# Optimization experiments

Hardware: AMD Instinct MI355X
Metric: run time of the kernel (lower is better)

The kernel has to match this reference:

```python
import jax, jax.numpy as jnp
import numpy as np

N_NODES = 4096
N_EDGES = 16384
L = 512
MP_STEPS = 5
DT = 0.01


def _mlp(x, W1, b1, W2, b2):
    return jax.nn.relu(x @ W1 + b1) @ W2 + b2


def _ln(x):
    m = jnp.mean(x, axis=-1, keepdims=True)
    v = jnp.var(x, axis=-1, keepdims=True)
    return (x - m) * jax.lax.rsqrt(v + 1e-6)


_PARAM_SHAPES = [
    ("enc_e_W1", (1, L)), ("enc_e_b1", (L,)), ("enc_e_W2", (L, L)), ("enc_e_b2", (L,)),
    ("enc_n_W1", (1, L)), ("enc_n_b1", (L,)), ("enc_n_W2", (L, L)), ("enc_n_b2", (L,)),
    ("proc_e_W1", (3 * L, L)), ("proc_e_b1", (L,)), ("proc_e_W2", (L, L)), ("proc_e_b2", (L,)),
    ("proc_n_W1", (2 * L, L)), ("proc_n_b1", (L,)), ("proc_n_W2", (L, L)), ("proc_n_b2", (L,)),
    ("dec_e_W1", (L, L)), ("dec_e_b1", (L,)), ("dec_e_W2", (L, 1)), ("dec_e_b2", (1,)),
]


def setup_inputs() -> dict:
    key = jax.random.key(0)
    ks = jax.random.split(key, 3 + len(_PARAM_SHAPES))
    d = {}
    d["state"] = jax.random.normal(ks[0], (N_EDGES + N_NODES,), dtype=jnp.float32)
    d["senders"] = jax.random.randint(ks[1], (N_EDGES,), 0, N_NODES)
    d["receivers"] = jax.random.randint(ks[2], (N_EDGES,), 0, N_NODES)
    for i, (name, shp) in enumerate(_PARAM_SHAPES):
        if name.endswith(("b1", "b2")):
            d[name] = jnp.zeros(shp, dtype=jnp.float32)
        else:
            d[name] = 0.02 * jax.random.normal(ks[3 + i], shp, dtype=jnp.float32)
    return d


def _hamiltonian(x, senders, receivers,
                 enc_e_W1, enc_e_b1, enc_e_W2, enc_e_b2,
                 enc_n_W1, enc_n_b1, enc_n_W2, enc_n_b2,
                 proc_e_W1, proc_e_b1, proc_e_W2, proc_e_b2,
                 proc_n_W1, proc_n_b1, proc_n_W2, proc_n_b2,
                 dec_e_W1, dec_e_b1, dec_e_W2, dec_e_b2):
    # graph_from_state: edge scalars then node scalars
    e = x[:N_EDGES].reshape(N_EDGES, 1)
    n = x[N_EDGES:].reshape(N_NODES, 1)
    # encode (MLP + layer norm)
    eh = _ln(_mlp(e, enc_e_W1, enc_e_b1, enc_e_W2, enc_e_b2))  # [E, L]
    nh = _ln(_mlp(n, enc_n_W1, enc_n_b1, enc_n_W2, enc_n_b2))  # [N, L]
    # process: num_mp_steps of GraphNetwork-style message passing, shared params
    for _ in range(MP_STEPS):
        msg_in = jnp.concatenate([eh, nh[senders], nh[receivers]], axis=-1)  # [E, 3L]
        eh = eh + _mlp(msg_in, proc_e_W1, proc_e_b1, proc_e_W2, proc_e_b2)
        agg = jax.ops.segment_sum(eh, receivers, num_segments=N_NODES)  # [N, L]
        node_in = jnp.concatenate([nh, agg], axis=-1)  # [N, 2L]
        nh = nh + _mlp(node_in, proc_n_W1, proc_n_b1, proc_n_W2, proc_n_b2)
    # decode edges to scalars; H = sum of decoded edge energies
    dec_e = _mlp(eh, dec_e_W1, dec_e_b1, dec_e_W2, dec_e_b2)  # [E, 1]
    return jnp.sum(dec_e)


def reference(state, senders, receivers,
              enc_e_W1, enc_e_b1, enc_e_W2, enc_e_b2,
              enc_n_W1, enc_n_b1, enc_n_W2, enc_n_b2,
              proc_e_W1, proc_e_b1, proc_e_W2, proc_e_b2,
              proc_n_W1, proc_n_b1, proc_n_W2, proc_n_b2,
              dec_e_W1, dec_e_b1, dec_e_W2, dec_e_b2):
    def H_fn(x):
        return _hamiltonian(x, senders, receivers,
                            enc_e_W1, enc_e_b1, enc_e_W2, enc_e_b2,
                            enc_n_W1, enc_n_b1, enc_n_W2, enc_n_b2,
                            proc_e_W1, proc_e_b1, proc_e_W2, proc_e_b2,
                            proc_n_W1, proc_n_b1, proc_n_W2, proc_n_b2,
                            dec_e_W1, dec_e_b1, dec_e_W2, dec_e_b2)
    H, dH = jax.value_and_grad(H_fn)(state)
    # one integrator step driven by the Hamiltonian gradient (stand-in for DAE solve)
    next_state = state - DT * dH
    return next_state
```

## Files before the change

### kernel.cpp

```cpp
#include <hip/hip_runtime.h>


#define E_ROWS 16384
#define N_ROWS 4096
#define ALL_ROWS 20480
#define DT_F   0.01f

typedef unsigned char u8;
typedef unsigned short u16;
typedef unsigned long long u64;
typedef __attribute__((ext_vector_type(8))) short short8v;
typedef __attribute__((ext_vector_type(4))) float f32x4;

__device__ __forceinline__ u16 f2b(float f) {
    union { float f; unsigned u; } v; v.f = f;
    unsigned r = v.u + 0x7FFF + ((v.u >> 16) & 1);
    return (u16)(r >> 16);
}
__device__ __forceinline__ float b2f(u16 u) {
    union { unsigned u; float f; } v; v.u = ((unsigned)u) << 16;
    return v.f;
}
__device__ __forceinline__ void gld16(const u16* g, u16* l) {
    __builtin_amdgcn_global_load_lds((const __attribute__((address_space(1))) void*)g,
                                     (__attribute__((address_space(3))) void*)l, 16, 0, 0);
}
template<int N> __device__ __forceinline__ void waitcnt_vm() {
    if constexpr (N == 0)      asm volatile("s_waitcnt vmcnt(0)" ::: "memory");
    else if constexpr (N == 2) asm volatile("s_waitcnt vmcnt(2)" ::: "memory");
    else if constexpr (N == 3) asm volatile("s_waitcnt vmcnt(3)" ::: "memory");
    else if constexpr (N == 4) asm volatile("s_waitcnt vmcnt(4)" ::: "memory");
    else if constexpr (N == 6) asm volatile("s_waitcnt vmcnt(6)" ::: "memory");
    else if constexpr (N == 8) asm volatile("s_waitcnt vmcnt(8)" ::: "memory");
}

template<int BM, int WM, int WN, int KTOT, int LDA, int LDC,
         bool ADD_C, bool GATHER2, bool BIAS, bool RELU_MASK, bool APPLY_MASK,
         bool WBF16, bool DUALOUT, bool ROWDOT, bool DECW2, bool BSEL>
__global__ __launch_bounds__(256)
void bgemm(const u16* __restrict__ A, const u16* __restrict__ Bt, const u16* __restrict__ Bt2,
           u16* __restrict__ Cb,
           const u16* __restrict__ Cinb, const float* __restrict__ bias,
           const float* __restrict__ bias2, const u16* __restrict__ G12b,
           const int* __restrict__ sidx, const int* __restrict__ ridx,
           u8* __restrict__ maskw, u16* __restrict__ C2b,
           const float* __restrict__ wvec, const float* __restrict__ wvec2,
           float* __restrict__ outp)
{
    constexpr int BN = WN * 64;
    constexpr int NA = BM / 16;
    constexpr int TC = (BM + BN) / 16;
    constexpr int PER = TC / 4;
    constexpr int NT = KTOT / 32;
    constexpr int IFRAG = BM / WM / 16;
    constexpr int BUFU = TC * 512;
    constexpr int LSZ = (3 * BUFU > BM * BN) ? 3 * BUFU : BM * BN;
    __shared__ u16 Ls[LSZ];

    const int tid = threadIdx.x;
    const int lane = tid & 63;
    const int wv = tid >> 6;
    const int wr = wv / WN;
    const int wc = wv % WN;

    const int gx = gridDim.x;
    int id = blockIdx.y * gx + blockIdx.x;
    const int nwg = gx * gridDim.y;
    id = (id & 7) * (nwg >> 3) + (id >> 3);
    const int bx = id % gx;
    const int by = id / gx;
    const int rowBase = by * BM;
    const int colBase = bx * BN;

    const u16* BtU = Bt;
    const float* biasU = bias;
    const float* wvecU = wvec;
    if (BSEL && rowBase >= E_ROWS) { BtU = Bt2; biasU = bias2; wvecU = wvec2; }

    const int srow = lane & 15;
    const int slotk = (lane >> 4) << 3;

    const u16* srcs[PER];
    int dstoff[PER];
#pragma unroll
    for (int q = 0; q < PER; ++q) {
        const int c = wv + (q << 2);
        if (c < NA)
            srcs[q] = A + (size_t)(rowBase + c * 16 + srow) * LDA + slotk;
        else
            srcs[q] = BtU + (size_t)(colBase + (c - NA) * 16 + srow) * KTOT + slotk;
        dstoff[q] = c * 512;
    }

    f32x4 acc[IFRAG][4];
#pragma unroll
    for (int i = 0; i < IFRAG; ++i)
#pragma unroll
        for (int j = 0; j < 4; ++j)
            acc[i][j] = (f32x4){0.f, 0.f, 0.f, 0.f};

    const int fro = ((lane >> 4) << 7) + ((lane & 15) << 3);

#pragma unroll
    for (int q = 0; q < PER; ++q) gld16(srcs[q], &Ls[dstoff[q]]);
#pragma unroll
    for (int q = 0; q < PER; ++q) gld16(srcs[q] + 32, &Ls[BUFU + dstoff[q]]);
    waitcnt_vm<PER>();
    __builtin_amdgcn_s_barrier();
    asm volatile("" ::: "memory");

    for (int t = 0; t < NT; ++t) {
        const int cur = t % 3;
        if (t + 2 < NT) {
            const int nxt = (t + 2) % 3;
#pragma unroll
            for (int q = 0; q < PER; ++q)
                gld16(srcs[q] + (t + 2) * 32, &Ls[nxt * BUFU + dstoff[q]]);
        }
        const u16* Lc = &Ls[cur * BUFU];
        short8v af[IFRAG], bfm[4];
#pragma unroll
        for (int i = 0; i < IFRAG; ++i)
            af[i] = *(const short8v*)&Lc[((wr * IFRAG + i) << 9) + fro];
#pragma unroll
        for (int j = 0; j < 4; ++j)
            bfm[j] = *(const short8v*)&Lc[((NA + (wc << 2) + j) << 9) + fro];
#pragma unroll
        for (int i = 0; i < IFRAG; ++i)
#pragma unroll
            for (int j = 0; j < 4; ++j)
                acc[i][j] = __builtin_amdgcn_mfma_f32_16x16x32_bf16(af[i], bfm[j], acc[i][j], 0, 0, 0);
        if (t + 1 < NT) {
            if (t + 2 < NT) waitcnt_vm<PER>();
            else            waitcnt_vm<0>();
            __builtin_amdgcn_s_barrier();
            asm volatile("" ::: "memory");
        }
    }
    __syncthreads();

    {
        const int colL = wc * 64 + (lane & 15);
        const int rowL0 = wr * (BM / WM) + ((lane >> 4) << 2);
#pragma unroll
        for (int i = 0; i < IFRAG; ++i)
#pragma unroll
            for (int r = 0; r < 4; ++r) {
                const int row = rowL0 + (i << 4) + r;
#pragma unroll
                for (int j = 0; j < 4; ++j) {
                    const int col = colL + (j << 4);
                    int byte = row * (BN * 2) + col * 2;
                    byte ^= (row & 7) << 4;
                    *(u16*)((char*)Ls + byte) = f2b(acc[i][j][r]);
                }
            }
        __syncthreads();

        constexpr int TPR = BN / 8;
        constexpr int RPP = 256 / TPR;
        constexpr int NP = BM / RPP;
        const int rloc = tid / TPR;
        const int seg = tid % TPR;
        const int col0 = seg * 8;
        const bool upper = DUALOUT && (colBase >= 512);
#pragma unroll
        for (int p = 0; p < NP; ++p) {
            const int row = p * RPP + rloc;
            const int grow = rowBase + row;
            const int gcol = colBase + col0;
            int byte = row * (BN * 2) + col0 * 2;
            byte ^= (row & 7) << 4;
            const short8v sv = *(const short8v*)((const char*)Ls + byte);
            float v[8];
#pragma unroll
            for (int e = 0; e < 8; ++e) v[e] = b2f((u16)sv[e]);

            if (DUALOUT && upper) {
                short8v res;
#pragma unroll
                for (int e = 0; e < 8; ++e) res[e] = (short)f2b(v[e]);
                *(short8v*)&C2b[(size_t)grow * 512 + (gcol - 512)] = res;
                continue;
            }
            if (GATHER2) {
                const int si = sidx[grow], ri = ridx[grow];
                const short8v g1 = *(const short8v*)&G12b[(size_t)si * 1024 + gcol];
                const short8v g2 = *(const short8v*)&G12b[(size_t)ri * 1024 + 512 + gcol];
#pragma unroll
                for (int e = 0; e < 8; ++e) v[e] += b2f((u16)g1[e]) + b2f((u16)g2[e]);
            }
            if (ADD_C) {
                const short8v c8 = *(const short8v*)&Cinb[(size_t)grow * LDC + gcol];
#pragma unroll
                for (int e = 0; e < 8; ++e) v[e] += b2f((u16)c8[e]);
            }
            if (BIAS) {
                const float4 b0 = *(const float4*)&biasU[gcol];
                const float4 b1 = *(const float4*)&biasU[gcol + 4];
                v[0] += b0.x; v[1] += b0.y; v[2] += b0.z; v[3] += b0.w;
                v[4] += b1.x; v[5] += b1.y; v[6] += b1.z; v[7] += b1.w;
            }
            if (DECW2) {
                const float4 w0 = *(const float4*)&wvecU[gcol];
                const float4 w1 = *(const float4*)&wvecU[gcol + 4];
                const float wl[8] = {w0.x, w0.y, w0.z, w0.w, w1.x, w1.y, w1.z, w1.w};
                short8v res;
#pragma unroll
                for (int e = 0; e < 8; ++e) res[e] = (v[e] > 0.f) ? (short)f2b(wl[e]) : (short)0;
                *(short8v*)&Cb[(size_t)grow * LDC + gcol] = res;
                continue;
            }
            if (RELU_MASK) {
                u64 mm = 0;
#pragma unroll
                for (int e = 0; e < 8; ++e) {
                    const bool m = v[e] > 0.f;
                    mm |= (u64)(m ? 1 : 0) << (e * 8);
                    if (!m) v[e] = 0.f;
                }
                *(u64*)&maskw[(size_t)grow * 512 + gcol] = mm;
            }
            if (APPLY_MASK) {
                const u64 mm = *(const u64*)&maskw[(size_t)grow * 512 + gcol];
#pragma unroll
                for (int e = 0; e < 8; ++e)
                    if (!((mm >> (e * 8)) & 0xff)) v[e] = 0.f;
            }
            if (ROWDOT) {
                const float4 w0 = *(const float4*)&wvecU[gcol];
                const float4 w1 = *(const float4*)&wvecU[gcol + 4];
                float rds = v[0] * w0.x + v[1] * w0.y + v[2] * w0.z + v[3] * w0.w
                          + v[4] * w1.x + v[5] * w1.y + v[6] * w1.z + v[7] * w1.w;
#pragma unroll
                for (int m = 1; m < TPR; m <<= 1) rds += __shfl_xor(rds, m);
                if (seg == 0) atomicAdd(outp + grow, -DT_F * rds);
            }
            if (WBF16) {
                short8v res;
#pragma unroll
                for (int e = 0; e < 8; ++e) res[e] = (short)f2b(v[e]);
                *(short8v*)&Cb[(size_t)grow * LDC + gcol] = res;
            }
        }
    }
}

struct WArgs {
    const float* src[10];
    u16* dstP[10];
    u16* dstT[10];
    int ldP[10], ldT[10];
};

__global__ void wcvt_kernel(WArgs a)
{
    const int i = blockIdx.z;
    const float* W = a.src[i];
    u16* P = a.dstP[i]; const int lp = a.ldP[i];
    u16* T = a.dstT[i]; const int lt = a.ldT[i];
    __shared__ u16 t[64][66];
    const int rb = blockIdx.y << 6, cb = blockIdx.x << 6;
    const int tr = threadIdx.x >> 4;
    const int tc = (threadIdx.x & 15) << 2;
#pragma unroll
    for (int rr = 0; rr < 4; ++rr) {
        const int r = tr + (rr << 4);
        const float4 v = *(const float4*)&W[(size_t)(rb + r) * 512 + cb + tc];
        ushort4 u; u.x = f2b(v.x); u.y = f2b(v.y); u.z = f2b(v.z); u.w = f2b(v.w);
        *(ushort4*)&P[(size_t)(rb + r) * lp + cb + tc] = u;
        t[r][tc] = u.x; t[r][tc + 1] = u.y; t[r][tc + 2] = u.z; t[r][tc + 3] = u.w;
    }
    __syncthreads();
#pragma unroll
    for (int rr = 0; rr < 4; ++rr) {
        const int n = tr + (rr << 4);
        ushort4 u;
        u.x = t[tc][n]; u.y = t[tc + 1][n]; u.z = t[tc + 2][n]; u.w = t[tc + 3][n];
        *(ushort4*)&T[(size_t)(cb + n) * lt + rb + tc] = u;
    }
}

__device__ void csr_build(const int* __restrict__ idx, int* __restrict__ starts,
                          int* __restrict__ eids)
{
    __shared__ int hist[4096];
    __shared__ int scanbuf[1024];
    const int t = threadIdx.x;
    for (int i = t; i < 4096; i += 1024) hist[i] = 0;
    __syncthreads();
    for (int e = t; e < 16384; e += 1024) atomicAdd(&hist[idx[e]], 1);
    __syncthreads();
    const int base = t << 2;
    const int l0 = hist[base], l1 = hist[base + 1], l2 = hist[base + 2], l3 = hist[base + 3];
    const int lsum = l0 + l1 + l2 + l3;
    scanbuf[t] = lsum;
    __syncthreads();
    for (int ofs = 1; ofs < 1024; ofs <<= 1) {
        const int v = scanbuf[t];
        const int u = (t >= ofs) ? scanbuf[t - ofs] : 0;
        __syncthreads();
        scanbuf[t] = v + u;
        __syncthreads();
    }
    const int excl = scanbuf[t] - lsum;
    const int p0 = excl, p1 = p0 + l0, p2 = p1 + l1, p3 = p2 + l2;
    starts[base] = p0; starts[base + 1] = p1; starts[base + 2] = p2; starts[base + 3] = p3;
    if (t == 0) starts[4096] = 16384;
    __syncthreads();
    hist[base] = p0; hist[base + 1] = p1; hist[base + 2] = p2; hist[base + 3] = p3;
    __syncthreads();
    for (int e = t; e < 16384; e += 1024) {
        const int pos = atomicAdd(&hist[idx[e]], 1);
        eids[pos] = e;
    }
    __syncthreads();
    for (int n = t; n < 4096; n += 1024) {
        const int s0 = starts[n], s1 = hist[n];
        for (int i = s0 + 1; i < s1; ++i) {
            const int v = eids[i];
            int j = i - 1;
            while (j >= s0 && eids[j] > v) { eids[j + 1] = eids[j]; --j; }
            eids[j + 1] = v;
        }
    }
}

__global__ __launch_bounds__(1024) void csr2_kernel(const int* __restrict__ senders,
                                                    const int* __restrict__ receivers,
                                                    int* __restrict__ sst, int* __restrict__ seid,
                                                    int* __restrict__ rst, int* __restrict__ reid)
{
    if (blockIdx.x == 0) csr_build(receivers, rst, reid);
    else                 csr_build(senders, sst, seid);
}

__global__ void init_out_kernel(const float* __restrict__ state, float* __restrict__ out)
{
    const int t = blockIdx.x * 256 + threadIdx.x;
    out[t] = state[t];
}

__global__ void seg_agg_fwd_kernel(const u16* __restrict__ ehb, const int* __restrict__ starts,
                                   const int* __restrict__ eids, const u16* __restrict__ nhb,
                                   u16* __restrict__ nagg)
{
    const int n = blockIdx.x, c = threadIdx.x;
    const int s0 = starts[n], s1 = starts[n + 1];
    float a0 = 0.f, a1 = 0.f;
    for (int i = s0; i < s1; ++i) {
        const u16* p = ehb + (size_t)eids[i] * 512;
        a0 += b2f(p[c]); a1 += b2f(p[c + 256]);
    }
    u16* d = nagg + (size_t)n * 1024;
    const u16* s = nhb + (size_t)n * 512;
    d[c] = s[c]; d[c + 256] = s[c + 256];
    d[512 + c] = f2b(a0); d[768 + c] = f2b(a1);
}

__global__ void seg_sr_bwd_kernel(const u16* __restrict__ dh1e,
                                  const int* __restrict__ sst, const int* __restrict__ seid,
                                  const int* __restrict__ rst, const int* __restrict__ reid,
                                  u16* __restrict__ SR)
{
    const int n = blockIdx.x, c = threadIdx.x;
    float a0 = 0.f, a1 = 0.f, b0 = 0.f, b1 = 0.f;
    for (int i = sst[n]; i < sst[n + 1]; ++i) {
        const u16* p = dh1e + (size_t)seid[i] * 512;
        a0 += b2f(p[c]); a1 += b2f(p[c + 256]);
    }
    for (int i = rst[n]; i < rst[n + 1]; ++i) {
        const u16* p = dh1e + (size_t)reid[i] * 512;
        b0 += b2f(p[c]); b1 += b2f(p[c + 256]);
    }
    u16* d = SR + (size_t)n * 1024;
    d[c] = f2b(a0); d[c + 256] = f2b(a1);
    d[512 + c] = f2b(b0); d[768 + c] = f2b(b1);
}

__global__ void enc_h1_kernel(const float* __restrict__ x,
                              const float* __restrict__ W1e, const float* __restrict__ b1e,
                              const float* __restrict__ W1n, const float* __restrict__ b1n,
                              u16* __restrict__ h1b, u8* __restrict__ mask)
{
    const int idx = blockIdx.x * 256 + threadIdx.x;
    const int row = idx >> 7;
    const int c = (idx & 127) << 2;
    const bool edge = row < E_ROWS;
    const float* W1 = edge ? W1e : W1n;
    const float* b1 = edge ? b1e : b1n;
    const float xv = x[row];
    const float4 w = *(const float4*)&W1[c];
    const float4 b = *(const float4*)&b1[c];
    float4 v;
    v.x = fmaf(xv, w.x, b.x); v.y = fmaf(xv, w.y, b.y);
    v.z = fmaf(xv, w.z, b.z); v.w = fmaf(xv, w.w, b.w);
    uchar4 m;
    m.x = v.x > 0.f; m.y = v.y > 0.f; m.z = v.z > 0.f; m.w = v.w > 0.f;
    v.x = m.x ? v.x : 0.f; v.y = m.y ? v.y : 0.f;
    v.z = m.z ? v.z : 0.f; v.w = m.w ? v.w : 0.f;
    const size_t o = (size_t)row * 512 + c;
    ushort4 u; u.x = f2b(v.x); u.y = f2b(v.y); u.z = f2b(v.z); u.w = f2b(v.w);
    *(ushort4*)&h1b[o] = u;
    *(uchar4*)&mask[o] = m;
}

__global__ void ln_fwd_kernel(u16* __restrict__ x, u16* __restrict__ xhat_b,
                              float* __restrict__ rstd_save)
{
    const int row = blockIdx.x, tid = threadIdx.x;
    u16* p = x + (size_t)row * 512;
    const float a = b2f(p[tid]), b = b2f(p[tid + 256]);
    __shared__ float s1[256], s2[256];
    s1[tid] = a + b; s2[tid] = a * a + b * b;
    __syncthreads();
    for (int d = 128; d > 0; d >>= 1) {
        if (tid < d) { s1[tid] += s1[tid + d]; s2[tid] += s2[tid + d]; }
        __syncthreads();
    }
    const float mean = s1[0] * (1.f / 512.f);
    const float var = s2[0] * (1.f / 512.f) - mean * mean;
    const float r = rsqrtf(var + 1e-6f);
    const u16 ya = f2b((a - mean) * r), yb = f2b((b - mean) * r);
    p[tid] = ya; p[tid + 256] = yb;
    xhat_b[(size_t)row * 512 + tid] = ya;
    xhat_b[(size_t)row * 512 + tid + 256] = yb;
    if (tid == 0) rstd_save[row] = r;
}

__global__ void ln_bwd_kernel(u16* __restrict__ d, const u16* __restrict__ xhat_b,
                              const float* __restrict__ rstd)
{
    const int row = blockIdx.x, tid = threadIdx.x;
    u16* p = d + (size_t)row * 512;
    const u16* xh = xhat_b + (size_t)row * 512;
    const float da = b2f(p[tid]), dbv = b2f(p[tid + 256]);
    const float xa = b2f(xh[tid]), xbv = b2f(xh[tid + 256]);
    __shared__ float s1[256], s2[256];
    s1[tid] = da + dbv; s2[tid] = da * xa + dbv * xbv;
    __syncthreads();
    for (int dd = 128; dd > 0; dd >>= 1) {
        if (tid < dd) { s1[tid] += s1[tid + dd]; s2[tid] += s2[tid + dd]; }
        __syncthreads();
    }
    const float m1 = s1[0] * (1.f / 512.f);
    const float m2 = s2[0] * (1.f / 512.f);
    const float r = rstd[row];
    p[tid] = f2b(r * (da - m1 - xa * m2));
    p[tid + 256] = f2b(r * (dbv - m1 - xbv * m2));
}

__global__ void gather_add_kernel(u16* __restrict__ dst, const u16* __restrict__ src,
                                  const int* __restrict__ idx)
{
    const int t = blockIdx.x * 256 + threadIdx.x;
    const int row = t >> 6;
    const int c = (t & 63) << 3;
    const size_t o = (size_t)row * 512 + c;
    short8v a = *(const short8v*)&dst[o];
    const short8v g = *(const short8v*)&src[(size_t)idx[row] * 512 + c];
    short8v r;
#pragma unroll
    for (int i = 0; i < 8; ++i)
        r[i] = (short)f2b(b2f((u16)a[i]) + b2f((u16)g[i]));
    *(short8v*)&dst[o] = r;
}

extern "C" void kernel_launch(void* const* d_in, const int* in_sizes, int n_in,
                              void* d_out, int out_size, void* d_ws, size_t ws_size,
                              hipStream_t stream)
{
    (void)in_sizes; (void)n_in; (void)out_size; (void)ws_size;
    const float* state     = (const float*)d_in[0];
    const int*   senders   = (const int*)d_in[1];
    const int*   receivers = (const int*)d_in[2];
    const float* enc_e_W1 = (const float*)d_in[3];
    const float* enc_e_b1 = (const float*)d_in[4];
    const float* enc_e_W2 = (const float*)d_in[5];
    const float* enc_e_b2 = (const float*)d_in[6];
    const float* enc_n_W1 = (const float*)d_in[7];
    const float* enc_n_b1 = (const float*)d_in[8];
    const float* enc_n_W2 = (const float*)d_in[9];
    const float* enc_n_b2 = (const float*)d_in[10];
    const float* pe_W1 = (const float*)d_in[11];
    const float* pe_b1 = (const float*)d_in[12];
    const float* pe_W2 = (const float*)d_in[13];
    const float* pe_b2 = (const float*)d_in[14];
    const float* pn_W1 = (const float*)d_in[15];
    const float* pn_b1 = (const float*)d_in[16];
    const float* pn_W2 = (const float*)d_in[17];
    const float* pn_b2 = (const float*)d_in[18];
    const float* de_W1 = (const float*)d_in[19];
    const float* de_b1 = (const float*)d_in[20];
    const float* de_W2 = (const float*)d_in[21];
    float* out = (float*)d_out;

    const size_t EL = (size_t)E_ROWS * 512, NL = (size_t)N_ROWS * 512;
    const size_t AL = (size_t)ALL_ROWS * 512;
    const size_t LL = 512 * 512;
    char* w = (char*)d_ws;
    size_t off = 0;
    auto carve = [&](size_t bytes) -> char* {
        char* p = w + off;
        off += (bytes + 255) & ~(size_t)255;
        return p;
    };
    u16* wb = (u16*)carve(20 * LL * 2);
    u16* WT0 = wb;           u16* WT1 = wb + LL;      u16* WT2 = wb + 2 * LL;
    u16* WT34 = wb + 3 * LL;                          u16* WT5 = wb + 5 * LL;
    u16* WT8 = wb + 6 * LL;  u16* WT9 = wb + 7 * LL;
    u16* WP0 = wb + 8 * LL;  u16* WP1 = wb + 9 * LL;  u16* WP2 = wb + 10 * LL;
    u16* WP5 = wb + 11 * LL; u16* WP8 = wb + 12 * LL; u16* WP9 = wb + 13 * LL;
    u16* WT67 = wb + 14 * LL;
    u16* WP34c = wb + 16 * LL;
    u16* WP67 = wb + 18 * LL;

    u16* ehb   = (u16*)carve(EL * 2);
    u16* nhb   = (u16*)carve(NL * 2);
    u16* h1eb  = (u16*)carve(EL * 2);
    u16* h1nb  = (u16*)carve(NL * 2);
    u16* eh0b  = (u16*)carve(EL * 2);
    u16* nh0b  = (u16*)carve(NL * 2);
    u8* menc   = (u8*)carve(AL);
    u16* G1b   = (u16*)carve(NL * 2);
    u16* G12b  = (u16*)carve(NL * 2 * 2);
    u16* nsr   = (u16*)carve(NL * 2 * 2);
    float* rstd = (float*)carve(ALL_ROWS * 4);
    u8* mpe    = (u8*)carve(5 * EL);
    u8* mpn    = (u8*)carve(5 * NL);
    int* rst  = (int*)carve(4097 * 4);
    int* reid = (int*)carve(16384 * 4);
    int* sst  = (int*)carve(4097 * 4);
    int* seid = (int*)carve(16384 * 4);

    const dim3 blk(256);
    const dim3 gE(4, E_ROWS / 128);
    const dim3 gA(4, ALL_ROWS / 128);
    const dim3 gN512(8, N_ROWS / 64);
    const dim3 gN1024(16, N_ROWS / 64);
    const float* fp = nullptr;
    u16* up = nullptr;
    const u16* cup = nullptr;
    const int* ip = nullptr;
    u8* mp = nullptr;
    float* f2p = nullptr;

    WArgs wa;
    const float* wsrc[10] = { enc_e_W2, enc_n_W2, pe_W1, pe_W1 + LL, pe_W1 + 2 * LL,
                              pe_W2, pn_W1, pn_W1 + LL, pn_W2, de_W1 };
    u16* dstP[10] = { WP0, WP1, WP2, WP34c, WP34c + 512, WP5, WP67, WP67 + LL, WP8, WP9 };
    int  ldP [10] = { 512, 512, 512, 1024,  1024,        512, 512,  512,       512, 512 };
    u16* dstT[10] = { WT0, WT1, WT2, WT34, WT34 + LL, WT5, WT67, WT67 + 512, WT8, WT9 };
    int  ldT [10] = { 512, 512, 512, 512,  512,       512, 1024, 1024,       512, 512 };
    for (int i = 0; i < 10; ++i) {
        wa.src[i] = wsrc[i]; wa.dstP[i] = dstP[i]; wa.dstT[i] = dstT[i];
        wa.ldP[i] = ldP[i]; wa.ldT[i] = ldT[i];
    }
    wcvt_kernel<<<dim3(8, 8, 10), blk, 0, stream>>>(wa);

    csr2_kernel<<<2, 1024, 0, stream>>>(senders, receivers, sst, seid, rst, reid);
    init_out_kernel<<<ALL_ROWS / 256, blk, 0, stream>>>(state, out);

    enc_h1_kernel<<<ALL_ROWS * 128 / 256, blk, 0, stream>>>(state, enc_e_W1, enc_e_b1,
                                                            enc_n_W1, enc_n_b1, h1eb, menc);
    bgemm<128,2,2,512,512,512, false,false,true,false,false, true,false,false,false,true>
        <<<gA, blk, 0, stream>>>(h1eb, WT0, WT1, ehb, cup, enc_e_b2, enc_n_b2, cup, ip, ip, mp, up, fp, fp, f2p);
    ln_fwd_kernel<<<ALL_ROWS, blk, 0, stream>>>(ehb, eh0b, rstd);

    for (int k = 0; k < 5; ++k) {
        bgemm<64,4,1,512,512,1024, false,false,false,false,false, true,false,false,false,false>
            <<<gN1024, blk, 0, stream>>>(nhb, WT34, cup, G12b, cup, fp, fp, cup, ip, ip, mp, up, fp, fp, f2p);
        bgemm<128,2,2,512,512,512, false,true,true,true,false, true,false,false,false,false>
            <<<gE, blk, 0, stream>>>(ehb, WT2, cup, h1eb, cup, pe_b1, fp, G12b, senders, receivers, mpe + (size_t)k * EL, up, fp, fp, f2p);
        bgemm<128,2,2,512,512,512, true,false,true,false,false, true,false,false,false,false>
            <<<gE, blk, 0, stream>>>(h1eb, WT5, cup, ehb, ehb, pe_b2, fp, cup, ip, ip, mp, up, fp, fp, f2p);
        seg_agg_fwd_kernel<<<N_ROWS, blk, 0, stream>>>(ehb, rst, reid, nhb, nsr);
        bgemm<64,4,1,1024,1024,512, false,false,true,true,false, true,false,false,false,false>
            <<<gN512, blk, 0, stream>>>(nsr, WT67, cup, h1nb, cup, pn_b1, fp, cup, ip, ip, mpn + (size_t)k * NL, up, fp, fp, f2p);
        bgemm<64,4,1,512,512,512, true,false,true,false,false, true,false,false,false,false>
            <<<gN512, blk, 0, stream>>>(h1nb, WT8, cup, nhb, nhb, pn_b2, fp, cup, ip, ip, mp, up, fp, fp, f2p);
    }

    bgemm<128,2,2,512,512,512, false,false,true,false,false, false,false,false,true,false>
        <<<gE, blk, 0, stream>>>(ehb, WT9, cup, h1eb, cup, de_b1, fp, cup, ip, ip, mp, up, de_W2, fp, f2p);

    bgemm<128,2,2,512,512,512, false,false,false,false,false, true,false,false,false,false>
        <<<gE, blk, 0, stream>>>(h1eb, WP9, cup, ehb, cup, fp, fp, cup, ip, ip, mp, up, fp, fp, f2p);

    for (int k = 4; k >= 0; --k) {
        if (k < 4) {
            bgemm<64,4,1,512,512,512, false,false,false,false,true, true,false,false,false,false>
                <<<gN512, blk, 0, stream>>>(nhb, WP8, cup, h1nb, cup, fp, fp, cup, ip, ip, mpn + (size_t)k * NL, up, fp, fp, f2p);
            bgemm<64,4,1,512,512,512, true,false,false,false,false, true,true,false,false,false>
                <<<gN1024, blk, 0, stream>>>(h1nb, WP67, cup, nhb, nhb, fp, fp, cup, ip, ip, mp, G1b, fp, fp, f2p);
            gather_add_kernel<<<E_ROWS * 64 / 256, blk, 0, stream>>>(ehb, G1b, receivers);
        }
        bgemm<128,2,2,512,512,512, false,false,false,false,true, true,false,false,false,false>
            <<<gE, blk, 0, stream>>>(ehb, WP5, cup, h1eb, cup, fp, fp, cup, ip, ip, mpe + (size_t)k * EL, up, fp, fp, f2p);
        bgemm<128,2,2,512,512,512, true,false,false,false,false, true,false,false,false,false>
            <<<gE, blk, 0, stream>>>(h1eb, WP2, cup, ehb, ehb, fp, fp, cup, ip, ip, mp, up, fp, fp, f2p);
        seg_sr_bwd_kernel<<<N_ROWS, blk, 0, stream>>>(h1eb, sst, seid, rst, reid, nsr);
        if (k == 4)
            bgemm<64,4,1,1024,1024,512, false,false,false,false,false, true,false,false,false,false>
                <<<gN512, blk, 0, stream>>>(nsr, WP34c, cup, nhb, cup, fp, fp, cup, ip, ip, mp, up, fp, fp, f2p);
        else
            bgemm<64,4,1,1024,1024,512, true,false,false,false,false, true,false,false,false,false>
                <<<gN512, blk, 0, stream>>>(nsr, WP34c, cup, nhb, nhb, fp, fp, cup, ip, ip, mp, up, fp, fp, f2p);
    }

    ln_bwd_kernel<<<ALL_ROWS, blk, 0, stream>>>(ehb, eh0b, rstd);
    bgemm<128,2,2,512,512,512, false,false,false,false,true, false,false,true,false,true>
        <<<gA, blk, 0, stream>>>(ehb, WP0, WP1, up, cup, fp, fp, cup, ip, ip, menc, up, enc_e_W1, enc_n_W1, out);
}
```

Baseline: 1.241 ms.

## Give each wave private double-buffered LDS tiles and drop per-step block barriers

```diff
diff --git a/kernel.cpp b/kernel.cpp
--- a/kernel.cpp
+++ b/kernel.cpp
@@ -27,10 +27,7 @@
 }
 template<int N> __device__ __forceinline__ void waitcnt_vm() {
     if constexpr (N == 0)      asm volatile("s_waitcnt vmcnt(0)" ::: "memory");
-    else if constexpr (N == 2) asm volatile("s_waitcnt vmcnt(2)" ::: "memory");
-    else if constexpr (N == 3) asm volatile("s_waitcnt vmcnt(3)" ::: "memory");
-    else if constexpr (N == 4) asm volatile("s_waitcnt vmcnt(4)" ::: "memory");
-    else if constexpr (N == 6) asm volatile("s_waitcnt vmcnt(6)" ::: "memory");
+    else if constexpr (N == 5) asm volatile("s_waitcnt vmcnt(5)" ::: "memory");
     else if constexpr (N == 8) asm volatile("s_waitcnt vmcnt(8)" ::: "memory");
 }
 
@@ -48,13 +45,12 @@
            float* __restrict__ outp)
 {
     constexpr int BN = WN * 64;
-    constexpr int NA = BM / 16;
-    constexpr int TC = (BM + BN) / 16;
-    constexpr int PER = TC / 4;
+    constexpr int NAW = BM / WM / 16;
+    constexpr int PERW = NAW + 4;
+    constexpr int WBUF = PERW * 512;
     constexpr int NT = KTOT / 32;
-    constexpr int IFRAG = BM / WM / 16;
-    constexpr int BUFU = TC * 512;
-    constexpr int LSZ = (3 * BUFU > BM * BN) ? 3 * BUFU : BM * BN;
+    constexpr int IFRAG = NAW;
+    constexpr int LSZ = (8 * WBUF > BM * BN) ? 8 * WBUF : BM * BN;
     __shared__ u16 Ls[LSZ];
 
     const int tid = threadIdx.x;
@@ -80,17 +76,15 @@
     const int srow = lane & 15;
     const int slotk = (lane >> 4) << 3;
 
-    const u16* srcs[PER];
-    int dstoff[PER];
-#pragma unroll
-    for (int q = 0; q < PER; ++q) {
-        const int c = wv + (q << 2);
-        if (c < NA)
-            srcs[q] = A + (size_t)(rowBase + c * 16 + srow) * LDA + slotk;
+    const u16* srcs[PERW];
+#pragma unroll
+    for (int q = 0; q < PERW; ++q) {
+        if (q < NAW)
+            srcs[q] = A + (size_t)(rowBase + wr * (BM / WM) + q * 16 + srow) * LDA + slotk;
         else
-            srcs[q] = BtU + (size_t)(colBase + (c - NA) * 16 + srow) * KTOT + slotk;
-        dstoff[q] = c * 512;
-    }
+            srcs[q] = BtU + (size_t)(colBase + wc * 64 + (q - NAW) * 16 + srow) * KTOT + slotk;
+    }
+    u16* Lw = Ls + wv * 2 * WBUF;
 
     f32x4 acc[IFRAG][4];
 #pragma unroll
@@ -102,40 +96,31 @@
     const int fro = ((lane >> 4) << 7) + ((lane & 15) << 3);
 
 #pragma unroll
-    for (int q = 0; q < PER; ++q) gld16(srcs[q], &Ls[dstoff[q]]);
-#pragma unroll
-    for (int q = 0; q < PER; ++q) gld16(srcs[q] + 32, &Ls[BUFU + dstoff[q]]);
-    waitcnt_vm<PER>();
-    __builtin_amdgcn_s_barrier();
-    asm volatile("" ::: "memory");
+    for (int q = 0; q < PERW; ++q) gld16(srcs[q], Lw + q * 512);
 
     for (int t = 0; t < NT; ++t) {
-        const int cur = t % 3;
-        if (t + 2 < NT) {
-            const int nxt = (t + 2) % 3;
-#pragma unroll
-            for (int q = 0; q < PER; ++q)
-                gld16(srcs[q] + (t + 2) * 32, &Ls[nxt * BUFU + dstoff[q]]);
+        if (t + 1 < NT) {
+            u16* Ln = Lw + ((t + 1) & 1) * WBUF;
+#pragma unroll
+            for (int q = 0; q < PERW; ++q)
+                gld16(srcs[q] + (t + 1) * 32, Ln + q * 512);
+            waitcnt_vm<PERW>();
+        } else {
+            waitcnt_vm<0>();
         }
-        const u16* Lc = &Ls[cur * BUFU];
+        const u16* Lc = Lw + (t & 1) * WBUF;
         short8v af[IFRAG], bfm[4];
 #pragma unroll
         for (int i = 0; i < IFRAG; ++i)
-            af[i] = *(const short8v*)&Lc[((wr * IFRAG + i) << 9) + fro];
+            af[i] = *(const short8v*)&Lc[(i << 9) + fro];
 #pragma unroll
         for (int j = 0; j < 4; ++j)
-            bfm[j] = *(const short8v*)&Lc[((NA + (wc << 2) + j) << 9) + fro];
+            bfm[j] = *(const short8v*)&Lc[((NAW + j) << 9) + fro];
 #pragma unroll
         for (int i = 0; i < IFRAG; ++i)
 #pragma unroll
             for (int j = 0; j < 4; ++j)
                 acc[i][j] = __builtin_amdgcn_mfma_f32_16x16x32_bf16(af[i], bfm[j], acc[i][j], 0, 0, 0);
-        if (t + 1 < NT) {
-            if (t + 2 < NT) waitcnt_vm<PER>();
-            else            waitcnt_vm<0>();
-            __builtin_amdgcn_s_barrier();
-            asm volatile("" ::: "memory");
-        }
     }
     __syncthreads();
 
```

Result: slower. 2.019 ms (+62.7%).
